# Optimization experiments

Hardware: AMD Instinct MI355X
Metric: run time of the kernel (lower is better)

Reference implementation:

```python
import jax, jax.numpy as jnp
import numpy as np

VN, BN, NSW, EC, MN = 64, 200, 10, 63, 73
FIN, HID = 32, 64
VLOW, VUPP = 0.9, 1.1


def _ln(z, eps=1e-5):
    m = jnp.mean(z, axis=-1, keepdims=True)
    v = jnp.var(z, axis=-1, keepdims=True)
    return (z - m) * jax.lax.rsqrt(v + eps)


def _layer(x, s, conn, deg_inv, Ws, Wi, Wj, U, Vw, first):
    # dense gated edge update over (B,V,V,H)
    e = jnp.einsum('bvwh,hk->bvwk', s, Ws) + (x @ Wi)[:, :, None, :] + (x @ Wj)[:, None, :, :]
    e = jax.nn.relu(_ln(e))
    s_out = e if first else s + e
    gate = jax.nn.sigmoid(s_out) * conn[None, :, :, None]
    msg = jnp.einsum('bvwh,bwh->bvh', gate, x @ Vw) * deg_inv[None, :, None]  # mean agg
    h = jax.nn.relu(_ln(x @ U + msg))
    return (h if first else x + h), s_out


def setup_inputs() -> dict:
    key = jax.random.key(0)
    ks = jax.random.split(key, 24)
    # radial feeder: path graph (line edges) + long-range tie switches, i<j (triu)
    ea = np.stack([np.arange(VN - 1), np.arange(1, VN)]).astype(np.int32)
    es = np.stack([np.arange(NSW), np.arange(NSW) + 32]).astype(np.int32)
    A = np.zeros((VN, VN), np.float32); A[ea[0], ea[1]] = 1; A[ea[1], ea[0]] = 1
    S = np.zeros((VN, VN), np.float32); S[es[0], es[1]] = 1; S[es[1], es[0]] = 1
    par = np.concatenate([ea[0], es[0]]); chi = np.concatenate([ea[1], es[1]])
    Incp = np.zeros((VN, MN), np.float32); Incp[par, np.arange(MN)] = 1
    Incc = np.zeros((VN, MN), np.float32); Incc[chi, np.arange(MN)] = 1
    deg = (A + S).sum(1)
    Dinv = np.diag((1.0 / np.maximum(deg, 1.0)).astype(np.float32))

    def w(k, shape):
        return jax.random.normal(k, shape, jnp.float32) / np.sqrt(shape[-2])

    return {
        'x': jax.random.normal(ks[0], (BN, VN, FIN), jnp.float32),
        'A': jnp.asarray(A), 'S': jnp.asarray(S),
        'embed_s': jax.random.normal(ks[1], (2, FIN), jnp.float32),
        'p0_Ws': w(ks[2], (FIN, HID)), 'p0_Wi': w(ks[3], (FIN, HID)),
        'p0_Wj': w(ks[4], (FIN, HID)), 'p0_U': w(ks[5], (FIN, HID)),
        'p0_V': w(ks[6], (FIN, HID)),
        'pl_Ws': w(ks[7], (2, HID, HID)), 'pl_Wi': w(ks[8], (2, HID, HID)),
        'pl_Wj': w(ks[9], (2, HID, HID)), 'pl_U': w(ks[10], (2, HID, HID)),
        'pl_V': w(ks[11], (2, HID, HID)),
        'smlp_W1': w(ks[12], (4 * HID, 4 * HID)), 'smlp_W2': w(ks[13], (4 * HID, 4)),
        'cmlp_W1': w(ks[14], (3 * HID, 3 * HID)), 'cmlp_W2': w(ks[15], (3 * HID, 3)),
        'Dinv': jnp.asarray(Dinv), 'Incp': jnp.asarray(Incp), 'Incc': jnp.asarray(Incc),
        'edge_A': jnp.asarray(ea), 'edge_S': jnp.asarray(es),
    }


def reference(x, A, S, embed_s, p0_Ws, p0_Wi, p0_Wj, p0_U, p0_V,
              pl_Ws, pl_Wi, pl_Wj, pl_U, pl_V,
              smlp_W1, smlp_W2, cmlp_W1, cmlp_W2,
              Dinv, Incp, Incc, edge_A, edge_S):
    B = x.shape[0]
    conn = jnp.clip(A + S, 0.0, 1.0)                       # (V,V) union adjacency
    deg_inv = 1.0 / jnp.maximum(conn.sum(1), 1.0)
    # init_embed_edges over dense S -> (B,V,V,FIN)
    s = jnp.broadcast_to(embed_s[S.astype(jnp.int32)][None], (B, VN, VN, FIN))
    xh, s = _layer(x, s, conn, deg_inv, p0_Ws, p0_Wi, p0_Wj, p0_U, p0_V, True)
    for l in range(pl_Ws.shape[0]):
        xh, s = _layer(xh, s, conn, deg_inv, pl_Ws[l], pl_Wi[l], pl_Wj[l], pl_U[l], pl_V[l], False)
    x_g = xh.sum(1)                                        # (B,H) graph feature

    # -- switch head (gather at triu switch edges, identical across batch) --
    si, sj = edge_S[0], edge_S[1]
    xg_s = jnp.broadcast_to(x_g[:, None, :], (B, si.shape[0], HID))
    smlp_in = jnp.concatenate([s[:, si, sj, :], xh[:, si], xh[:, sj], xg_s], axis=-1)
    smlp_out = jax.nn.sigmoid(jax.nn.relu(smlp_in @ smlp_W1) @ smlp_W2)  # (B,nsw,4)
    topology = smlp_out[..., 0]
    graph_topo = jnp.concatenate([jnp.ones((B, MN - NSW), x.dtype), topology], axis=1)
    ps = smlp_out[..., 1] - 0.5
    vs_p = VLOW * (1 - smlp_out[..., 2]) + VUPP * smlp_out[..., 2]
    vs_c = VLOW * (1 - smlp_out[..., 3]) + VUPP * smlp_out[..., 3]

    # -- connection head (gather at triu line edges) --
    ai, aj = edge_A[0], edge_A[1]
    xg_c = jnp.broadcast_to(x_g[:, None, :], (B, ai.shape[0], HID))
    cmlp_in = jnp.concatenate([xh[:, ai], xh[:, aj], xg_c], axis=-1)
    cmlp_out = jax.nn.sigmoid(jax.nn.relu(cmlp_in @ cmlp_W1) @ cmlp_W2)  # (B,Ec,3)
    pc = cmlp_out[..., 0] - 0.5
    vc_p = VLOW * (1 - cmlp_out[..., 1]) + VUPP * cmlp_out[..., 1]
    vc_c = VLOW * (1 - cmlp_out[..., 2]) + VUPP * cmlp_out[..., 2]

    # scatter into (B,M) physics tensors: first M-nsw cols from CMLP, last nsw from SMLP
    p_flow = jnp.concatenate([pc, ps], axis=1)
    v_par = jnp.concatenate([vc_p, vs_p], axis=1)
    v_chi = jnp.concatenate([vc_c, vs_c], axis=1)
    v = v_par @ (Dinv @ Incp).T + v_chi @ (Dinv @ Incc).T   # (B,V)
    v = v.at[:, 0].set(1.0)
    return jnp.concatenate([p_flow, v, graph_topo], axis=1)  # (B, M+V+M)
```

## Files before the change

kernel.cpp:

```cpp
#include <hip/hip_runtime.h>

#define BN 200
#define VN 64
#define HIDD 64
#define FINN 32
#define NSW 10
#define EC 63
#define MNE 73
#define NEDGE 146
#define NPACK 256

typedef unsigned short u16;
typedef unsigned int u32;
typedef _Float16 f16;
typedef __attribute__((ext_vector_type(8))) _Float16 f16x8;
typedef __attribute__((ext_vector_type(4))) float f32x4;

__device__ __forceinline__ float bfu(u16 u) { return __uint_as_float(((u32)u) << 16); }
__device__ __forceinline__ u16 f2bf(float f) {
    u32 x = __float_as_uint(f);
    u32 r = x + 0x7fffu + ((x >> 16) & 1u);
    return (u16)(r >> 16);
}
__device__ __forceinline__ float cvtv(const void* p, int i, int fl) {
    return fl ? bfu(((const u16*)p)[i]) : ((const float*)p)[i];
}
__device__ __forceinline__ int rfl(int v) { return __builtin_amdgcn_readfirstlane(v); }

__device__ __forceinline__ int swzp(int row, int col) { return col ^ ((row & 7) << 2); }
__device__ __forceinline__ int swz16(int row, int col) { return col ^ ((row & 7) << 3); }

__device__ __forceinline__ float ldh(const u16* P, int i) {
    union { u16 u; f16 h; } c; c.u = P[i];
    return (float)c.h;
}
__device__ __forceinline__ void sth(u16* P, int i, float f) {
    union { u16 u; f16 h; } c; c.h = (f16)f;
    P[i] = c.u;
}
__device__ __forceinline__ u16 f2h(float f) {
    union { u16 u; f16 h; } c; c.h = (f16)f;
    return c.u;
}
__device__ __forceinline__ f16x8 ldfragh(const u16* P, int i0) {
    return *(const f16x8*)&P[i0];
}

template <int CTRL>
__device__ __forceinline__ float dppadd(float x) {
    int v = __builtin_amdgcn_update_dpp(0, __float_as_int(x), CTRL, 0xf, 0xf, 1);
    return x + __int_as_float(v);
}
__device__ __forceinline__ float rl63(float x) {
    return __int_as_float(__builtin_amdgcn_readlane(__float_as_int(x), 63));
}

__device__ __forceinline__ void ln4_dpp(float ea, float eb, float ec, float ed,
                                        float& ra, float& rb, float& rc, float& rd) {
    float a1 = ea, b1 = eb, c1 = ec, d1 = ed;
    float a2 = ea * ea, b2 = eb * eb, c2 = ec * ec, d2 = ed * ed;
#define LSTEP(C) a1 = dppadd<C>(a1); b1 = dppadd<C>(b1); c1 = dppadd<C>(c1); d1 = dppadd<C>(d1); \
                 a2 = dppadd<C>(a2); b2 = dppadd<C>(b2); c2 = dppadd<C>(c2); d2 = dppadd<C>(d2);
    LSTEP(0x111) LSTEP(0x112) LSTEP(0x114) LSTEP(0x118) LSTEP(0x142) LSTEP(0x143)
#undef LSTEP
    float s1a = rl63(a1), s2a = rl63(a2);
    float s1b = rl63(b1), s2b = rl63(b2);
    float s1c = rl63(c1), s2c = rl63(c2);
    float s1d = rl63(d1), s2d = rl63(d2);
    float ma = s1a * 0.015625f, mb = s1b * 0.015625f;
    float mc = s1c * 0.015625f, md = s1d * 0.015625f;
    float va = fmaxf(s2a * 0.015625f - ma * ma, 0.f);
    float vb = fmaxf(s2b * 0.015625f - mb * mb, 0.f);
    float vc = fmaxf(s2c * 0.015625f - mc * mc, 0.f);
    float vd = fmaxf(s2d * 0.015625f - md * md, 0.f);
    ra = fmaxf((ea - ma) * rsqrtf(va + 1e-5f), 0.f);
    rb = fmaxf((eb - mb) * rsqrtf(vb + 1e-5f), 0.f);
    rc = fmaxf((ec - mc) * rsqrtf(vc + 1e-5f), 0.f);
    rd = fmaxf((ed - md) * rsqrtf(vd + 1e-5f), 0.f);
}

__device__ __forceinline__ float sigm(float x) {
    return __fdividef(1.f, 1.f + __expf(-x));
}

struct CvtArgs { const void* src[21]; };

__global__ __launch_bounds__(256) void k_prep(CvtArgs ca, const int* __restrict__ eA,
                                              const int* __restrict__ eS,
                                              u16* __restrict__ c1p, u16* __restrict__ c2p,
                                              u16* __restrict__ s1p, u16* __restrict__ s2p,
                                              u16* __restrict__ w0p, u16* __restrict__ wlp,
                                              float* __restrict__ ews, float* __restrict__ dinv,
                                              int* __restrict__ row_ptr, int* __restrict__ colp,
                                              int* __restrict__ sw_eidx,
                                              float* __restrict__ dinvD, int* __restrict__ incCnt,
                                              int* __restrict__ incM) {
    int t = threadIdx.x;
    int fl = (((const u16*)ca.src[1])[1] == 0x3F80) ? 1 : 0;
    if (blockIdx.x == 0) {
        __shared__ unsigned char flagL[64 * 65];
        __shared__ float wsL[FINN * 64];
        __shared__ float emL[64];
        __shared__ int degL[64], rpS[65], colS[NEDGE + 16];
        __shared__ int eAL[2 * EC], eSL[2 * NSW];

        if (t < 2 * EC) eAL[t] = eA[t];
        if (t >= 128 && t < 128 + 2 * NSW) eSL[t - 128] = eS[t - 128];
        if (t >= 160 && t < 224) emL[t - 160] = cvtv(ca.src[3], t - 160, fl);
        for (int i = t; i < FINN * 64; i += 256) wsL[i] = cvtv(ca.src[4], i, fl);
        for (int i = t; i < 4096; i += 256) {
            float a = cvtv(ca.src[1], i, fl);
            float s = cvtv(ca.src[2], i, fl);
            int r = i >> 6, c = i & 63;
            flagL[r * 65 + c] = (unsigned char)(((a != 0.f || s != 0.f) ? 1 : 0) |
                                                ((s != 0.f) ? 2 : 0));
        }
        __syncthreads();

        if (t < 128) {
            int j = t >> 6, k = t & 63;
            float a = 0.f;
#pragma unroll
            for (int h = 0; h < FINN; h++) a += emL[j * FINN + h] * wsL[h * 64 + k];
            ews[(j << 6) + k] = a;
        }
        if (t < 64) {
            int d = 0;
#pragma unroll
            for (int w = 0; w < 64; w++) d += flagL[t * 65 + w] & 1;
            degL[t] = d;
            dinv[t] = 1.f / fmaxf((float)d, 1.f);
        }
        __syncthreads();
        if (t == 0) {
            int c = 0;
            for (int v = 0; v < 64; v++) { rpS[v] = c; c += degL[v]; }
            rpS[64] = c;
        }
        __syncthreads();
        if (t < 65) row_ptr[t] = rpS[t];
        if (t < 64) {
            int pos = rpS[t];
#pragma unroll
            for (int w = 0; w < 64; w++) {
                int f = flagL[t * 65 + w];
                if (f & 1) colS[pos++] = w | ((f & 2) ? 256 : 0) | (t << 16);
            }
        }
        __syncthreads();
        int tot = rpS[64];
        if (t < tot) colp[t] = colS[t];
        if (t < NSW) {
            int si = eSL[t], sj = eSL[NSW + t];
            int idx = 0;
            for (int e = rpS[si]; e < rpS[si + 1]; e++)
                if ((colS[e] & 255) == sj) idx = e;
            sw_eidx[t] = idx;
        }
        if (t < 64) {
            dinvD[t] = cvtv(ca.src[18], t * 64 + t, fl);
            int cnt = 0;
            for (int m = 0; m < MNE; m++) {
                int par = (m < EC) ? eAL[m] : eSL[m - EC];
                int chi = (m < EC) ? eAL[EC + m] : eSL[NSW + (m - EC)];
                if (par == t && cnt < 8) incM[t * 8 + cnt++] = (m << 1);
                if (chi == t && cnt < 8) incM[t * 8 + cnt++] = (m << 1) | 1;
            }
            incCnt[t] = cnt;
        }
    } else {
        const int T1 = 36864, T2 = T1 + 3072, T3 = T2 + 65536, T4 = T3 + 4096;
        const int T5 = T4 + 8192, TOT = T5 + 40960;
        for (int i = (blockIdx.x - 1) * 256 + t; i < TOT; i += NPACK * 256) {
            int idx = i;
            const void* src;
            u16* dp;
            int K2, N2, nt, rem, loff = 0;
            if (idx < T1) {
                nt = idx / 3072; rem = idx - nt * 3072; src = ca.src[16];
                dp = c1p + idx; K2 = 192; N2 = 192;
            } else if (idx < T2) {
                idx -= T1; nt = 0; rem = idx; src = ca.src[17];
                dp = c2p + idx; K2 = 192; N2 = 3;
            } else if (idx < T3) {
                idx -= T2; nt = idx >> 12; rem = idx & 4095; src = ca.src[14];
                dp = s1p + idx; K2 = 256; N2 = 256;
            } else if (idx < T4) {
                idx -= T3; nt = 0; rem = idx; src = ca.src[15];
                dp = s2p + idx; K2 = 256; N2 = 4;
            } else if (idx < T5) {
                int j = idx - T4;
                int mt = j >> 11;
                int m2 = j & 2047;
                nt = m2 >> 9; rem = m2 & 511; src = ca.src[5 + mt];
                dp = w0p + j; K2 = 32; N2 = 64;
            } else {
                int j = idx - T5;
                int l = j / 20480;
                int jj = j - l * 20480;
                int mt = jj >> 12;
                int m2 = jj & 4095;
                nt = m2 >> 10; rem = m2 & 1023; src = ca.src[9 + mt];
                loff = l * 4096;
                dp = wlp + j; K2 = 64; N2 = 64;
            }
            int kb = rem >> 9, r8 = rem & 511, ln = r8 >> 3, jq = r8 & 7;
            int k = kb * 32 + ((ln >> 4) << 3) + jq;
            int n = nt * 16 + (ln & 15);
            float val = 0.f;
            if (n < N2 && k < K2) val = cvtv(src, loff + k * N2 + n, fl);
            *dp = f2h(val);
        }
    }
}

#define XI 0
#define XJ 1
#define XU 2
#define XV 3

__global__ __launch_bounds__(1024) void k_main(
    const void* __restrict__ xraw, const u16* __restrict__ A_u16,
    const int* __restrict__ eA, const int* __restrict__ eS,
    const float* __restrict__ ews, const float* __restrict__ dinv,
    const int* __restrict__ row_ptr, const int* __restrict__ colp,
    const int* __restrict__ sw_eidx,
    const float* __restrict__ dinvD, const int* __restrict__ incCnt, const int* __restrict__ incM,
    const u16* __restrict__ w0p, const u16* __restrict__ wlp,
    const u16* __restrict__ c1p, const u16* __restrict__ c2p,
    const u16* __restrict__ s1p, const u16* __restrict__ s2p,
    void* __restrict__ out_v)
{
    __shared__ __align__(16) u16 xPh[64 * 64];
    __shared__ __align__(16) u16 sPh[NEDGE * 64];
    __shared__ __align__(16) float preL[NEDGE * 64];
    __shared__ __align__(16) float tLs[4 * 64 * 64];
    __shared__ __align__(16) u16 xg16[64];
    __shared__ float ewsL[128];
    __shared__ float dinvL[64];
    __shared__ int rpL[65];
    __shared__ int colL[NEDGE + 6];
    __shared__ int swLx[NSW];
    __shared__ int eALs[2 * EC], eSLs[2 * NSW];
    __shared__ float cmoL[EC * 3], smoL[NSW * 4];

    int b = blockIdx.x, t = threadIdx.x;
    int lane = t & 63, wid = t >> 6;
    int m = lane & 15, quad = lane >> 4;
    int fl = (A_u16[1] == 0x3F80) ? 1 : 0;

    for (int i = t; i < 2048; i += 1024) {
        int r = i >> 5, c = i & 31;
        sth(xPh, (r << 6) + swz16(r, c), cvtv(xraw, b * 2048 + i, fl));
    }
    if (t < 128) ewsL[t] = ews[t];
    if (t < 64) dinvL[t] = dinv[t];
    if (t < 65) rpL[t] = row_ptr[t];
    if (t < NEDGE) colL[t] = colp[t];
    if (t < NSW) swLx[t] = sw_eidx[t];
    if (t >= 256 && t < 256 + 2 * EC) eALs[t - 256] = eA[t - 256];
    if (t >= 512 && t < 512 + 2 * NSW) eSLs[t - 512] = eS[t - 512];
    __syncthreads();

    {
        int mat = wid >> 2, Mt = wid & 3;
        const u16* bp = w0p + mat * 2048;
        int row = Mt * 16 + m;
        f16x8 a = ldfragh(xPh, (row << 6) + swz16(row, quad * 8));
        f32x4 acc[4];
#pragma unroll
        for (int nt = 0; nt < 4; nt++) {
            f16x8 bfr = ldfragh(bp, (nt << 9) + (lane << 3));
            acc[nt] = __builtin_amdgcn_mfma_f32_16x16x32_f16(a, bfr, (f32x4){0.f, 0.f, 0.f, 0.f}, 0, 0, 0);
        }
#pragma unroll
        for (int nt = 0; nt < 4; nt++)
#pragma unroll
            for (int r = 0; r < 4; r++) {
                int orow = Mt * 16 + quad * 4 + r;
                tLs[mat * 4096 + (orow << 6) + swzp(orow, nt * 16 + m)] = acc[nt][r];
            }
    }
    __syncthreads();

    for (int base = 0; base < NEDGE; base += 64) {
        int e0 = base + wid;
        int e1i = e0 + 16, e2i = e0 + 32, e3i = e0 + 48;
        int ok1 = e1i < NEDGE, ok2 = e2i < NEDGE, ok3 = e3i < NEDGE;
        int f1 = ok1 ? e1i : e0, f2 = ok2 ? e2i : e0, f3 = ok3 ? e3i : e0;
        int cp0 = rfl(colL[e0]), cp1 = rfl(colL[f1]);
        int cp2 = rfl(colL[f2]), cp3 = rfl(colL[f3]);
        int w0 = cp0 & 255, v0 = (cp0 >> 16) & 255;
        int w1 = cp1 & 255, v1 = (cp1 >> 16) & 255;
        int w2 = cp2 & 255, v2 = (cp2 >> 16) & 255;
        int w3 = cp3 & 255, v3 = (cp3 >> 16) & 255;
        int h0i = (e0 << 6) + swz16(e0, lane);
        int h1i = (f1 << 6) + swz16(f1, lane);
        int h2i = (f2 << 6) + swz16(f2, lane);
        int h3i = (f3 << 6) + swz16(f3, lane);
        int p0i = (e0 << 6) + swzp(e0, lane);
        int p1i = (f1 << 6) + swzp(f1, lane);
        int p2i = (f2 << 6) + swzp(f2, lane);
        int p3i = (f3 << 6) + swzp(f3, lane);
        float ee0 = ewsL[(((cp0 >> 8) & 1) << 6) + lane]
                  + tLs[XI * 4096 + (v0 << 6) + swzp(v0, lane)]
                  + tLs[XJ * 4096 + (w0 << 6) + swzp(w0, lane)];
        float ee1 = ewsL[(((cp1 >> 8) & 1) << 6) + lane]
                  + tLs[XI * 4096 + (v1 << 6) + swzp(v1, lane)]
                  + tLs[XJ * 4096 + (w1 << 6) + swzp(w1, lane)];
        float ee2 = ewsL[(((cp2 >> 8) & 1) << 6) + lane]
                  + tLs[XI * 4096 + (v2 << 6) + swzp(v2, lane)]
                  + tLs[XJ * 4096 + (w2 << 6) + swzp(w2, lane)];
        float ee3 = ewsL[(((cp3 >> 8) & 1) << 6) + lane]
                  + tLs[XI * 4096 + (v3 << 6) + swzp(v3, lane)]
                  + tLs[XJ * 4096 + (w3 << 6) + swzp(w3, lane)];
        float h0, h1, h2, h3;
        ln4_dpp(ee0, ee1, ee2, ee3, h0, h1, h2, h3);
        sth(sPh, h0i, h0);
        preL[p0i] = tLs[XV * 4096 + (w0 << 6) + swzp(w0, lane)] * sigm(h0);
        if (ok1) {
            sth(sPh, h1i, h1);
            preL[p1i] = tLs[XV * 4096 + (w1 << 6) + swzp(w1, lane)] * sigm(h1);
        }
        if (ok2) {
            sth(sPh, h2i, h2);
            preL[p2i] = tLs[XV * 4096 + (w2 << 6) + swzp(w2, lane)] * sigm(h2);
        }
        if (ok3) {
            sth(sPh, h3i, h3);
            preL[p3i] = tLs[XV * 4096 + (w3 << 6) + swzp(w3, lane)] * sigm(h3);
        }
    }
    __syncthreads();

    {
        int v0 = wid << 2;
        int r0 = rfl(rpL[v0]), r1 = rfl(rpL[v0 + 1]), r2 = rfl(rpL[v0 + 2]);
        int r3 = rfl(rpL[v0 + 3]), r4 = rfl(rpL[v0 + 4]);
        float mc0 = 0.f, mc1 = 0.f, mc2 = 0.f, mc3 = 0.f;
        for (int e = r0; e < r1; e++) mc0 += preL[(e << 6) + swzp(e, lane)];
        for (int e = r1; e < r2; e++) mc1 += preL[(e << 6) + swzp(e, lane)];
        for (int e = r2; e < r3; e++) mc2 += preL[(e << 6) + swzp(e, lane)];
        for (int e = r3; e < r4; e++) mc3 += preL[(e << 6) + swzp(e, lane)];
        float z0 = tLs[XU * 4096 + ((v0 + 0) << 6) + swzp(v0 + 0, lane)] + mc0 * dinvL[v0 + 0];
        float z1 = tLs[XU * 4096 + ((v0 + 1) << 6) + swzp(v0 + 1, lane)] + mc1 * dinvL[v0 + 1];
        float z2 = tLs[XU * 4096 + ((v0 + 2) << 6) + swzp(v0 + 2, lane)] + mc2 * dinvL[v0 + 2];
        float z3 = tLs[XU * 4096 + ((v0 + 3) << 6) + swzp(v0 + 3, lane)] + mc3 * dinvL[v0 + 3];
        float h0, h1, h2, h3;
        ln4_dpp(z0, z1, z2, z3, h0, h1, h2, h3);
        sth(xPh, ((v0 + 0) << 6) + swz16(v0 + 0, lane), h0);
        sth(xPh, ((v0 + 1) << 6) + swz16(v0 + 1, lane), h1);
        sth(xPh, ((v0 + 2) << 6) + swz16(v0 + 2, lane), h2);
        sth(xPh, ((v0 + 3) << 6) + swz16(v0 + 3, lane), h3);
    }
    __syncthreads();

    for (int l = 0; l < 2; l++) {
        {
            int mat = wid >> 2, Mt = wid & 3;
            const u16* bp = wlp + l * 20480 + (mat + 1) * 4096;
            int row = Mt * 16 + m;
            f32x4 acc[4];
#pragma unroll
            for (int nt = 0; nt < 4; nt++) acc[nt] = (f32x4){0.f, 0.f, 0.f, 0.f};
#pragma unroll
            for (int kb = 0; kb < 2; kb++) {
                f16x8 a = ldfragh(xPh, (row << 6) + swz16(row, kb * 32 + quad * 8));
#pragma unroll
                for (int nt = 0; nt < 4; nt++) {
                    f16x8 bfr = ldfragh(bp, (((nt << 1) + kb) << 9) + (lane << 3));
                    acc[nt] = __builtin_amdgcn_mfma_f32_16x16x32_f16(a, bfr, acc[nt], 0, 0, 0);
                }
            }
#pragma unroll
            for (int nt = 0; nt < 4; nt++)
#pragma unroll
                for (int r = 0; r < 4; r++) {
                    int orow = Mt * 16 + quad * 4 + r;
                    tLs[mat * 4096 + (orow << 6) + swzp(orow, nt * 16 + m)] = acc[nt][r];
                }

            const u16* sbp = wlp + l * 20480;
            for (int u = wid; u < 40; u += 16) {
                int rt = u >> 2, ntq = u & 3;
                int srow = rt * 16 + m;
                int ar = (srow > NEDGE - 1) ? (NEDGE - 1) : srow;
                f32x4 sacc = (f32x4){0.f, 0.f, 0.f, 0.f};
#pragma unroll
                for (int kb = 0; kb < 2; kb++) {
                    f16x8 a = ldfragh(sPh, (ar << 6) + swz16(ar, kb * 32 + quad * 8));
                    f16x8 bfr = ldfragh(sbp, (((ntq << 1) + kb) << 9) + (lane << 3));
                    sacc = __builtin_amdgcn_mfma_f32_16x16x32_f16(a, bfr, sacc, 0, 0, 0);
                }
#pragma unroll
                for (int r = 0; r < 4; r++) {
                    int orow = rt * 16 + quad * 4 + r;
                    if (orow < NEDGE)
                        preL[(orow << 6) + swzp(orow, ntq * 16 + m)] = sacc[r];
                }
            }
        }
        __syncthreads();

        for (int base = 0; base < NEDGE; base += 64) {
            int e0 = base + wid;
            int e1i = e0 + 16, e2i = e0 + 32, e3i = e0 + 48;
            int ok1 = e1i < NEDGE, ok2 = e2i < NEDGE, ok3 = e3i < NEDGE;
            int f1 = ok1 ? e1i : e0, f2 = ok2 ? e2i : e0, f3 = ok3 ? e3i : e0;
            int cp0 = rfl(colL[e0]), cp1 = rfl(colL[f1]);
            int cp2 = rfl(colL[f2]), cp3 = rfl(colL[f3]);
            int w0 = cp0 & 255, v0 = (cp0 >> 16) & 255;
            int w1 = cp1 & 255, v1 = (cp1 >> 16) & 255;
            int w2 = cp2 & 255, v2 = (cp2 >> 16) & 255;
            int w3 = cp3 & 255, v3 = (cp3 >> 16) & 255;
            int h0i = (e0 << 6) + swz16(e0, lane);
            int h1i = (f1 << 6) + swz16(f1, lane);
            int h2i = (f2 << 6) + swz16(f2, lane);
            int h3i = (f3 << 6) + swz16(f3, lane);
            int p0i = (e0 << 6) + swzp(e0, lane);
            int p1i = (f1 << 6) + swzp(f1, lane);
            int p2i = (f2 << 6) + swzp(f2, lane);
            int p3i = (f3 << 6) + swzp(f3, lane);
            float ee0 = preL[p0i]
                      + tLs[XI * 4096 + (v0 << 6) + swzp(v0, lane)]
                      + tLs[XJ * 4096 + (w0 << 6) + swzp(w0, lane)];
            float ee1 = preL[p1i]
                      + tLs[XI * 4096 + (v1 << 6) + swzp(v1, lane)]
                      + tLs[XJ * 4096 + (w1 << 6) + swzp(w1, lane)];
            float ee2 = preL[p2i]
                      + tLs[XI * 4096 + (v2 << 6) + swzp(v2, lane)]
                      + tLs[XJ * 4096 + (w2 << 6) + swzp(w2, lane)];
            float ee3 = preL[p3i]
                      + tLs[XI * 4096 + (v3 << 6) + swzp(v3, lane)]
                      + tLs[XJ * 4096 + (w3 << 6) + swzp(w3, lane)];
            float h0, h1, h2, h3;
            ln4_dpp(ee0, ee1, ee2, ee3, h0, h1, h2, h3);
            float s0 = ldh(sPh, h0i) + h0;
            sth(sPh, h0i, s0);
            preL[p0i] = tLs[XV * 4096 + (w0 << 6) + swzp(w0, lane)] * sigm(s0);
            if (ok1) {
                float s1v = ldh(sPh, h1i) + h1;
                sth(sPh, h1i, s1v);
                preL[p1i] = tLs[XV * 4096 + (w1 << 6) + swzp(w1, lane)] * sigm(s1v);
            }
            if (ok2) {
                float s2v = ldh(sPh, h2i) + h2;
                sth(sPh, h2i, s2v);
                preL[p2i] = tLs[XV * 4096 + (w2 << 6) + swzp(w2, lane)] * sigm(s2v);
            }
            if (ok3) {
                float s3v = ldh(sPh, h3i) + h3;
                sth(sPh, h3i, s3v);
                preL[p3i] = tLs[XV * 4096 + (w3 << 6) + swzp(w3, lane)] * sigm(s3v);
            }
        }
        __syncthreads();

        {
            int v0 = wid << 2;
            int r0 = rfl(rpL[v0]), r1 = rfl(rpL[v0 + 1]), r2 = rfl(rpL[v0 + 2]);
            int r3 = rfl(rpL[v0 + 3]), r4 = rfl(rpL[v0 + 4]);
            float mc0 = 0.f, mc1 = 0.f, mc2 = 0.f, mc3 = 0.f;
            for (int e = r0; e < r1; e++) mc0 += preL[(e << 6) + swzp(e, lane)];
            for (int e = r1; e < r2; e++) mc1 += preL[(e << 6) + swzp(e, lane)];
            for (int e = r2; e < r3; e++) mc2 += preL[(e << 6) + swzp(e, lane)];
            for (int e = r3; e < r4; e++) mc3 += preL[(e << 6) + swzp(e, lane)];
            float z0 = tLs[XU * 4096 + ((v0 + 0) << 6) + swzp(v0 + 0, lane)] + mc0 * dinvL[v0 + 0];
            float z1 = tLs[XU * 4096 + ((v0 + 1) << 6) + swzp(v0 + 1, lane)] + mc1 * dinvL[v0 + 1];
            float z2 = tLs[XU * 4096 + ((v0 + 2) << 6) + swzp(v0 + 2, lane)] + mc2 * dinvL[v0 + 2];
            float z3 = tLs[XU * 4096 + ((v0 + 3) << 6) + swzp(v0 + 3, lane)] + mc3 * dinvL[v0 + 3];
            float h0, h1, h2, h3;
            ln4_dpp(z0, z1, z2, z3, h0, h1, h2, h3);
            int i0 = ((v0 + 0) << 6) + swz16(v0 + 0, lane);
            int i1 = ((v0 + 1) << 6) + swz16(v0 + 1, lane);
            int i2 = ((v0 + 2) << 6) + swz16(v0 + 2, lane);
            int i3 = ((v0 + 3) << 6) + swz16(v0 + 3, lane);
            float x0 = ldh(xPh, i0) + h0;
            float x1 = ldh(xPh, i1) + h1;
            float x2 = ldh(xPh, i2) + h2;
            float x3 = ldh(xPh, i3) + h3;
            sth(xPh, i0, x0);
            sth(xPh, i1, x1);
            sth(xPh, i2, x2);
            sth(xPh, i3, x3);
            if (l == 1) tLs[(wid << 6) + lane] = x0 + x1 + x2 + x3;
        }
        __syncthreads();
    }

    if (t < 64) {
        float s = 0.f;
#pragma unroll
        for (int i = 0; i < 16; i++) s += tLs[(i << 6) + t];
        sth(xg16, t, s);
    }
    __syncthreads();

    u16* hcP = (u16*)tLs;
    u16* hsP = (u16*)tLs + 12288;

    if (wid < 12) {
        int Mt = wid & 3, ntg = wid >> 2;
        int e = Mt * 16 + m; if (e > 62) e = 62;
        int ai = eALs[e], aj = eALs[EC + e];
        f32x4 acc[4];
#pragma unroll
        for (int j = 0; j < 4; j++) acc[j] = (f32x4){0.f, 0.f, 0.f, 0.f};
#pragma unroll
        for (int kb = 0; kb < 6; kb++) {
            int k = kb * 32 + quad * 8;
            f16x8 a;
            if (k < 64) {
                a = ldfragh(xPh, (ai << 6) + swz16(ai, k));
            } else if (k < 128) {
                a = ldfragh(xPh, (aj << 6) + swz16(aj, k - 64));
            } else {
                a = ldfragh(xg16, k - 128);
            }
#pragma unroll
            for (int j = 0; j < 4; j++) {
                int nt = ntg * 4 + j;
                f16x8 bfr = ldfragh(c1p, ((nt * 6 + kb) << 9) + (lane << 3));
                acc[j] = __builtin_amdgcn_mfma_f32_16x16x32_f16(a, bfr, acc[j], 0, 0, 0);
            }
        }
#pragma unroll
        for (int j = 0; j < 4; j++) {
            int nt = ntg * 4 + j;
#pragma unroll
            for (int r = 0; r < 4; r++) {
                int row = Mt * 16 + quad * 4 + r;
                sth(hcP, row * 192 + swz16(row, nt * 16 + m), fmaxf(acc[j][r], 0.f));
            }
        }
    } else {
        int e2 = (m > 9) ? 9 : m;
        int si = eSLs[e2], sj = eSLs[NSW + e2];
        int sw = swLx[e2];
        f32x4 accS[4];
#pragma unroll
        for (int j = 0; j < 4; j++) accS[j] = (f32x4){0.f, 0.f, 0.f, 0.f};
#pragma unroll
        for (int kb = 0; kb < 8; kb++) {
            int k = kb * 32 + quad * 8;
            f16x8 a;
            if (k < 64) {
                a = ldfragh(sPh, (sw << 6) + swz16(sw, k));
            } else if (k < 128) {
                a = ldfragh(xPh, (si << 6) + swz16(si, k - 64));
            } else if (k < 192) {
                a = ldfragh(xPh, (sj << 6) + swz16(sj, k - 128));
            } else {
                a = ldfragh(xg16, k - 192);
            }
#pragma unroll
            for (int j = 0; j < 4; j++) {
                int nt = (wid - 12) * 4 + j;
                f16x8 bfr = ldfragh(s1p, ((nt * 8 + kb) << 9) + (lane << 3));
                accS[j] = __builtin_amdgcn_mfma_f32_16x16x32_f16(a, bfr, accS[j], 0, 0, 0);
            }
        }
#pragma unroll
        for (int j = 0; j < 4; j++) {
            int nt = (wid - 12) * 4 + j;
#pragma unroll
            for (int r = 0; r < 4; r++) {
                int row = quad * 4 + r;
                sth(hsP, (row << 8) + swz16(row, nt * 16 + m), fmaxf(accS[j][r], 0.f));
            }
        }
    }
    __syncthreads();

    if (wid < 4) {
        f32x4 accD = (f32x4){0.f, 0.f, 0.f, 0.f};
        int row = wid * 16 + m;
#pragma unroll
        for (int kb = 0; kb < 6; kb++) {
            f16x8 a = ldfragh(hcP, row * 192 + swz16(row, kb * 32 + quad * 8));
            f16x8 bfr = ldfragh(c2p, (kb << 9) + (lane << 3));
            accD = __builtin_amdgcn_mfma_f32_16x16x32_f16(a, bfr, accD, 0, 0, 0);
        }
#pragma unroll
        for (int r = 0; r < 4; r++) {
            int row2 = wid * 16 + quad * 4 + r;
            if (row2 < EC && m < 3)
                cmoL[row2 * 3 + m] = 1.f / (1.f + __expf(-accD[r]));
        }
    } else if (wid == 4) {
        f32x4 accT = (f32x4){0.f, 0.f, 0.f, 0.f};
#pragma unroll
        for (int kb = 0; kb < 8; kb++) {
            f16x8 a = ldfragh(hsP, (m << 8) + swz16(m, kb * 32 + quad * 8));
            f16x8 bfr = ldfragh(s2p, (kb << 9) + (lane << 3));
            accT = __builtin_amdgcn_mfma_f32_16x16x32_f16(a, bfr, accT, 0, 0, 0);
        }
#pragma unroll
        for (int r = 0; r < 4; r++) {
            int row = quad * 4 + r;
            if (row < NSW && m < 4)
                smoL[row * 4 + m] = 1.f / (1.f + __expf(-accT[r]));
        }
    }
    __syncthreads();

    if (t < 2 * MNE + VN) {
        float val;
        if (t < MNE) {
            val = (t < EC) ? cmoL[t * 3] - 0.5f : smoL[(t - EC) * 4 + 1] - 0.5f;
        } else if (t < MNE + VN) {
            int i = t - MNE;
            if (i == 0) {
                val = 1.0f;
            } else {
                float acc = 0.f;
                int c = incCnt[i];
                for (int q = 0; q < c; q++) {
                    int em = incM[i * 8 + q];
                    int mm = em >> 1, role = em & 1;
                    float vv = (mm < EC) ? 0.9f + 0.2f * cmoL[mm * 3 + 1 + role]
                                         : 0.9f + 0.2f * smoL[(mm - EC) * 4 + 2 + role];
                    acc += vv;
                }
                val = acc * dinvD[i];
            }
        } else {
            int mm = t - (MNE + VN);
            val = (mm < EC) ? 1.0f : smoL[(mm - EC) * 4];
        }
        size_t oidx = (size_t)b * (2 * MNE + VN) + t;
        if (fl) ((u16*)out_v)[oidx] = f2bf(val);
        else    ((float*)out_v)[oidx] = val;
    }
}

extern "C" void kernel_launch(void* const* d_in, const int* in_sizes, int n_in,
                              void* d_out, int out_size, void* d_ws, size_t ws_size,
                              hipStream_t stream) {
    const int* eA = (const int*)d_in[21];
    const int* eS = (const int*)d_in[22];

    float* pool = (float*)d_ws;
    float* ews     = pool;
    float* dinv    = ews + 128;
    float* dinvD   = dinv + 64;
    int*   row_ptr = (int*)(dinvD + 64);
    int*   colp    = row_ptr + 80;
    int*   sw_eidx = colp + 256;
    int*   incCnt  = sw_eidx + 16;
    int*   incM    = incCnt + 64;
    u16*   c1p = (u16*)(incM + 512);
    u16*   c2p = c1p + 36864;
    u16*   s1p = c2p + 3072;
    u16*   s2p = s1p + 65536;
    u16*   w0p = s2p + 4096;
    u16*   wlp = w0p + 8192;

    CvtArgs ca;
    for (int i = 0; i < 21; i++) ca.src[i] = d_in[i];

    k_prep<<<1 + NPACK, 256, 0, stream>>>(ca, eA, eS,
                                          c1p, c2p, s1p, s2p, w0p, wlp,
                                          ews, dinv, row_ptr, colp, sw_eidx,
                                          dinvD, incCnt, incM);

    k_main<<<BN, 1024, 0, stream>>>(d_in[0], (const u16*)d_in[1], eA, eS,
                                    ews, dinv, row_ptr, colp, sw_eidx,
                                    dinvD, incCnt, incM,
                                    w0p, wlp, c1p, c2p, s1p, s2p,
                                    d_out);
}
```

Baseline: 152.7 us.

## Process two channels per lane with half-wave edges and paired DPP layernorm

```diff
diff --git a/kernel.cpp b/kernel.cpp
--- a/kernel.cpp
+++ b/kernel.cpp
@@ -25,7 +25,6 @@
 __device__ __forceinline__ float cvtv(const void* p, int i, int fl) {
     return fl ? bfu(((const u16*)p)[i]) : ((const float*)p)[i];
 }
-__device__ __forceinline__ int rfl(int v) { return __builtin_amdgcn_readfirstlane(v); }
 
 __device__ __forceinline__ int swzp(int row, int col) { return col ^ ((row & 7) << 2); }
 __device__ __forceinline__ int swz16(int row, int col) { return col ^ ((row & 7) << 3); }
@@ -40,6 +39,14 @@
 }
 __device__ __forceinline__ u16 f2h(float f) {
     union { u16 u; f16 h; } c; c.h = (f16)f;
+    return c.u;
+}
+__device__ __forceinline__ void unp2(u32 w, float& a, float& b) {
+    union { u32 u; f16 h[2]; } c; c.u = w;
+    a = (float)c.h[0]; b = (float)c.h[1];
+}
+__device__ __forceinline__ u32 pk2(float a, float b) {
+    union { u32 u; f16 h[2]; } c; c.h[0] = (f16)a; c.h[1] = (f16)b;
     return c.u;
 }
 __device__ __forceinline__ f16x8 ldfragh(const u16* P, int i0) {
@@ -51,32 +58,27 @@
     int v = __builtin_amdgcn_update_dpp(0, __float_as_int(x), CTRL, 0xf, 0xf, 1);
     return x + __int_as_float(v);
 }
-__device__ __forceinline__ float rl63(float x) {
-    return __int_as_float(__builtin_amdgcn_readlane(__float_as_int(x), 63));
-}
-
-__device__ __forceinline__ void ln4_dpp(float ea, float eb, float ec, float ed,
-                                        float& ra, float& rb, float& rc, float& rd) {
-    float a1 = ea, b1 = eb, c1 = ec, d1 = ed;
-    float a2 = ea * ea, b2 = eb * eb, c2 = ec * ec, d2 = ed * ed;
-#define LSTEP(C) a1 = dppadd<C>(a1); b1 = dppadd<C>(b1); c1 = dppadd<C>(c1); d1 = dppadd<C>(d1); \
-                 a2 = dppadd<C>(a2); b2 = dppadd<C>(b2); c2 = dppadd<C>(c2); d2 = dppadd<C>(d2);
-    LSTEP(0x111) LSTEP(0x112) LSTEP(0x114) LSTEP(0x118) LSTEP(0x142) LSTEP(0x143)
-#undef LSTEP
-    float s1a = rl63(a1), s2a = rl63(a2);
-    float s1b = rl63(b1), s2b = rl63(b2);
-    float s1c = rl63(c1), s2c = rl63(c2);
-    float s1d = rl63(d1), s2d = rl63(d2);
-    float ma = s1a * 0.015625f, mb = s1b * 0.015625f;
-    float mc = s1c * 0.015625f, md = s1d * 0.015625f;
-    float va = fmaxf(s2a * 0.015625f - ma * ma, 0.f);
-    float vb = fmaxf(s2b * 0.015625f - mb * mb, 0.f);
-    float vc = fmaxf(s2c * 0.015625f - mc * mc, 0.f);
-    float vd = fmaxf(s2d * 0.015625f - md * md, 0.f);
-    ra = fmaxf((ea - ma) * rsqrtf(va + 1e-5f), 0.f);
-    rb = fmaxf((eb - mb) * rsqrtf(vb + 1e-5f), 0.f);
-    rc = fmaxf((ec - mc) * rsqrtf(vc + 1e-5f), 0.f);
-    rd = fmaxf((ed - md) * rsqrtf(vd + 1e-5f), 0.f);
+template <int N>
+__device__ __forceinline__ float rlN(float x) {
+    return __int_as_float(__builtin_amdgcn_readlane(__float_as_int(x), N));
+}
+
+__device__ __forceinline__ void lnpair(float p0, float p1, int isHi, float& o0, float& o1) {
+    float s1 = p0 + p1;
+    float s2 = fmaf(p0, p0, p1 * p1);
+    s1 = dppadd<0x111>(s1); s1 = dppadd<0x112>(s1); s1 = dppadd<0x114>(s1); s1 = dppadd<0x118>(s1);
+    s2 = dppadd<0x111>(s2); s2 = dppadd<0x112>(s2); s2 = dppadd<0x114>(s2); s2 = dppadd<0x118>(s2);
+    float a1 = rlN<15>(s1) + rlN<31>(s1);
+    float b1 = rlN<47>(s1) + rlN<63>(s1);
+    float a2 = rlN<15>(s2) + rlN<31>(s2);
+    float b2 = rlN<47>(s2) + rlN<63>(s2);
+    float S1 = isHi ? b1 : a1;
+    float S2 = isHi ? b2 : a2;
+    float mean = S1 * 0.015625f;
+    float var = fmaxf(S2 * 0.015625f - mean * mean, 0.f);
+    float rn = rsqrtf(var + 1e-5f);
+    o0 = fmaxf((p0 - mean) * rn, 0.f);
+    o1 = fmaxf((p1 - mean) * rn, 0.f);
 }
 
 __device__ __forceinline__ float sigm(float x) {
@@ -247,11 +249,22 @@
     int b = blockIdx.x, t = threadIdx.x;
     int lane = t & 63, wid = t >> 6;
     int m = lane & 15, quad = lane >> 4;
+    int half = lane >> 5, hl = lane & 31, c2 = hl << 1;
     int fl = (A_u16[1] == 0x3F80) ? 1 : 0;
 
-    for (int i = t; i < 2048; i += 1024) {
-        int r = i >> 5, c = i & 31;
-        sth(xPh, (r << 6) + swz16(r, c), cvtv(xraw, b * 2048 + i, fl));
+    {
+        int i2 = t << 1;
+        int r = i2 >> 5, c = i2 & 31;
+        float va, vb;
+        if (fl) {
+            u32 wv = ((const u32*)xraw)[(size_t)b * 1024 + t];
+            va = bfu((u16)(wv & 0xffffu));
+            vb = bfu((u16)(wv >> 16));
+        } else {
+            float2 f = ((const float2*)xraw)[(size_t)b * 1024 + t];
+            va = f.x; vb = f.y;
+        }
+        *(u32*)&xPh[(r << 6) + swz16(r, c)] = pk2(va, vb);
     }
     if (t < 128) ewsL[t] = ews[t];
     if (t < 64) dinvL[t] = dinv[t];
@@ -283,75 +296,51 @@
     }
     __syncthreads();
 
-    for (int base = 0; base < NEDGE; base += 64) {
-        int e0 = base + wid;
-        int e1i = e0 + 16, e2i = e0 + 32, e3i = e0 + 48;
-        int ok1 = e1i < NEDGE, ok2 = e2i < NEDGE, ok3 = e3i < NEDGE;
-        int f1 = ok1 ? e1i : e0, f2 = ok2 ? e2i : e0, f3 = ok3 ? e3i : e0;
-        int cp0 = rfl(colL[e0]), cp1 = rfl(colL[f1]);
-        int cp2 = rfl(colL[f2]), cp3 = rfl(colL[f3]);
-        int w0 = cp0 & 255, v0 = (cp0 >> 16) & 255;
-        int w1 = cp1 & 255, v1 = (cp1 >> 16) & 255;
-        int w2 = cp2 & 255, v2 = (cp2 >> 16) & 255;
-        int w3 = cp3 & 255, v3 = (cp3 >> 16) & 255;
-        int h0i = (e0 << 6) + swz16(e0, lane);
-        int h1i = (f1 << 6) + swz16(f1, lane);
-        int h2i = (f2 << 6) + swz16(f2, lane);
-        int h3i = (f3 << 6) + swz16(f3, lane);
-        int p0i = (e0 << 6) + swzp(e0, lane);
-        int p1i = (f1 << 6) + swzp(f1, lane);
-        int p2i = (f2 << 6) + swzp(f2, lane);
-        int p3i = (f3 << 6) + swzp(f3, lane);
-        float ee0 = ewsL[(((cp0 >> 8) & 1) << 6) + lane]
-                  + tLs[XI * 4096 + (v0 << 6) + swzp(v0, lane)]
-                  + tLs[XJ * 4096 + (w0 << 6) + swzp(w0, lane)];
-        float ee1 = ewsL[(((cp1 >> 8) & 1) << 6) + lane]
-                  + tLs[XI * 4096 + (v1 << 6) + swzp(v1, lane)]
-                  + tLs[XJ * 4096 + (w1 << 6) + swzp(w1, lane)];
-        float ee2 = ewsL[(((cp2 >> 8) & 1) << 6) + lane]
-                  + tLs[XI * 4096 + (v2 << 6) + swzp(v2, lane)]
-                  + tLs[XJ * 4096 + (w2 << 6) + swzp(w2, lane)];
-        float ee3 = ewsL[(((cp3 >> 8) & 1) << 6) + lane]
-                  + tLs[XI * 4096 + (v3 << 6) + swzp(v3, lane)]
-                  + tLs[XJ * 4096 + (w3 << 6) + swzp(w3, lane)];
-        float h0, h1, h2, h3;
-        ln4_dpp(ee0, ee1, ee2, ee3, h0, h1, h2, h3);
-        sth(sPh, h0i, h0);
-        preL[p0i] = tLs[XV * 4096 + (w0 << 6) + swzp(w0, lane)] * sigm(h0);
-        if (ok1) {
-            sth(sPh, h1i, h1);
-            preL[p1i] = tLs[XV * 4096 + (w1 << 6) + swzp(w1, lane)] * sigm(h1);
-        }
-        if (ok2) {
-            sth(sPh, h2i, h2);
-            preL[p2i] = tLs[XV * 4096 + (w2 << 6) + swzp(w2, lane)] * sigm(h2);
-        }
-        if (ok3) {
-            sth(sPh, h3i, h3);
-            preL[p3i] = tLs[XV * 4096 + (w3 << 6) + swzp(w3, lane)] * sigm(h3);
+    for (int base = 0; base < NEDGE; base += 128) {
+#pragma unroll
+        for (int s = 0; s < 4; s++) {
+            int q = (s << 1) + half;
+            int e = base + wid + (q << 4);
+            int ok = e < NEDGE;
+            int ec = ok ? e : (NEDGE - 1);
+            int cp = colL[ec];
+            int w = cp & 255, v = (cp >> 16) & 255;
+            float2 ew = *(const float2*)&ewsL[((((cp >> 8) & 1)) << 6) + c2];
+            float2 xi = *(const float2*)&tLs[XI * 4096 + (v << 6) + swzp(v, c2)];
+            float2 xj = *(const float2*)&tLs[XJ * 4096 + (w << 6) + swzp(w, c2)];
+            float p0 = ew.x + xi.x + xj.x;
+            float p1 = ew.y + xi.y + xj.y;
+            float h0, h1;
+            lnpair(p0, p1, half, h0, h1);
+            float2 xv = *(const float2*)&tLs[XV * 4096 + (w << 6) + swzp(w, c2)];
+            float2 g;
+            g.x = xv.x * sigm(h0);
+            g.y = xv.y * sigm(h1);
+            if (ok) {
+                *(u32*)&sPh[(ec << 6) + swz16(ec, c2)] = pk2(h0, h1);
+                *(float2*)&preL[(ec << 6) + swzp(ec, c2)] = g;
+            }
         }
     }
     __syncthreads();
 
     {
-        int v0 = wid << 2;
-        int r0 = rfl(rpL[v0]), r1 = rfl(rpL[v0 + 1]), r2 = rfl(rpL[v0 + 2]);
-        int r3 = rfl(rpL[v0 + 3]), r4 = rfl(rpL[v0 + 4]);
-        float mc0 = 0.f, mc1 = 0.f, mc2 = 0.f, mc3 = 0.f;
-        for (int e = r0; e < r1; e++) mc0 += preL[(e << 6) + swzp(e, lane)];
-        for (int e = r1; e < r2; e++) mc1 += preL[(e << 6) + swzp(e, lane)];
-        for (int e = r2; e < r3; e++) mc2 += preL[(e << 6) + swzp(e, lane)];
-        for (int e = r3; e < r4; e++) mc3 += preL[(e << 6) + swzp(e, lane)];
-        float z0 = tLs[XU * 4096 + ((v0 + 0) << 6) + swzp(v0 + 0, lane)] + mc0 * dinvL[v0 + 0];
-        float z1 = tLs[XU * 4096 + ((v0 + 1) << 6) + swzp(v0 + 1, lane)] + mc1 * dinvL[v0 + 1];
-        float z2 = tLs[XU * 4096 + ((v0 + 2) << 6) + swzp(v0 + 2, lane)] + mc2 * dinvL[v0 + 2];
-        float z3 = tLs[XU * 4096 + ((v0 + 3) << 6) + swzp(v0 + 3, lane)] + mc3 * dinvL[v0 + 3];
-        float h0, h1, h2, h3;
-        ln4_dpp(z0, z1, z2, z3, h0, h1, h2, h3);
-        sth(xPh, ((v0 + 0) << 6) + swz16(v0 + 0, lane), h0);
-        sth(xPh, ((v0 + 1) << 6) + swz16(v0 + 1, lane), h1);
-        sth(xPh, ((v0 + 2) << 6) + swz16(v0 + 2, lane), h2);
-        sth(xPh, ((v0 + 3) << 6) + swz16(v0 + 3, lane), h3);
+#pragma unroll
+        for (int s = 0; s < 2; s++) {
+            int v = (wid << 2) + (s << 1) + half;
+            int r0 = rpL[v], r1 = rpL[v + 1];
+            float m0 = 0.f, m1 = 0.f;
+            for (int e = r0; e < r1; e++) {
+                float2 p = *(const float2*)&preL[(e << 6) + swzp(e, c2)];
+                m0 += p.x; m1 += p.y;
+            }
+            float2 xu = *(const float2*)&tLs[XU * 4096 + (v << 6) + swzp(v, c2)];
+            float di = dinvL[v];
+            float z0 = xu.x + m0 * di, z1 = xu.y + m1 * di;
+            float h0, h1;
+            lnpair(z0, z1, half, h0, h1);
+            *(u32*)&xPh[(v << 6) + swz16(v, c2)] = pk2(h0, h1);
+        }
     }
     __syncthreads();
 
@@ -402,88 +391,65 @@
         }
         __syncthreads();
 
-        for (int base = 0; base < NEDGE; base += 64) {
-            int e0 = base + wid;
-            int e1i = e0 + 16, e2i = e0 + 32, e3i = e0 + 48;
-            int ok1 = e1i < NEDGE, ok2 = e2i < NEDGE, ok3 = e3i < NEDGE;
-            int f1 = ok1 ? e1i : e0, f2 = ok2 ? e2i : e0, f3 = ok3 ? e3i : e0;
-            int cp0 = rfl(colL[e0]), cp1 = rfl(colL[f1]);
-            int cp2 = rfl(colL[f2]), cp3 = rfl(colL[f3]);
-            int w0 = cp0 & 255, v0 = (cp0 >> 16) & 255;
-            int w1 = cp1 & 255, v1 = (cp1 >> 16) & 255;
-            int w2 = cp2 & 255, v2 = (cp2 >> 16) & 255;
-            int w3 = cp3 & 255, v3 = (cp3 >> 16) & 255;
-            int h0i = (e0 << 6) + swz16(e0, lane);
-            int h1i = (f1 << 6) + swz16(f1, lane);
-            int h2i = (f2 << 6) + swz16(f2, lane);
-            int h3i = (f3 << 6) + swz16(f3, lane);
-            int p0i = (e0 << 6) + swzp(e0, lane);
-            int p1i = (f1 << 6) + swzp(f1, lane);
-            int p2i = (f2 << 6) + swzp(f2, lane);
-            int p3i = (f3 << 6) + swzp(f3, lane);
-            float ee0 = preL[p0i]
-                      + tLs[XI * 4096 + (v0 << 6) + swzp(v0, lane)]
-                      + tLs[XJ * 4096 + (w0 << 6) + swzp(w0, lane)];
-            float ee1 = preL[p1i]
-                      + tLs[XI * 4096 + (v1 << 6) + swzp(v1, lane)]
-                      + tLs[XJ * 4096 + (w1 << 6) + swzp(w1, lane)];
-            float ee2 = preL[p2i]
-                      + tLs[XI * 4096 + (v2 << 6) + swzp(v2, lane)]
-                      + tLs[XJ * 4096 + (w2 << 6) + swzp(w2, lane)];
-            float ee3 = preL[p3i]
-                      + tLs[XI * 4096 + (v3 << 6) + swzp(v3, lane)]
-                      + tLs[XJ * 4096 + (w3 << 6) + swzp(w3, lane)];
-            float h0, h1, h2, h3;
-            ln4_dpp(ee0, ee1, ee2, ee3, h0, h1, h2, h3);
-            float s0 = ldh(sPh, h0i) + h0;
-            sth(sPh, h0i, s0);
-            preL[p0i] = tLs[XV * 4096 + (w0 << 6) + swzp(w0, lane)] * sigm(s0);
-            if (ok1) {
-                float s1v = ldh(sPh, h1i) + h1;
-                sth(sPh, h1i, s1v);
-                preL[p1i] = tLs[XV * 4096 + (w1 << 6) + swzp(w1, lane)] * sigm(s1v);
-            }
-            if (ok2) {
-                float s2v = ldh(sPh, h2i) + h2;
-                sth(sPh, h2i, s2v);
-                preL[p2i] = tLs[XV * 4096 + (w2 << 6) + swzp(w2, lane)] * sigm(s2v);
-            }
-            if (ok3) {
-                float s3v = ldh(sPh, h3i) + h3;
-                sth(sPh, h3i, s3v);
-                preL[p3i] = tLs[XV * 4096 + (w3 << 6) + swzp(w3, lane)] * sigm(s3v);
+        for (int base = 0; base < NEDGE; base += 128) {
+#pragma unroll
+            for (int s = 0; s < 4; s++) {
+                int q = (s << 1) + half;
+                int e = base + wid + (q << 4);
+                int ok = e < NEDGE;
+                int ec = ok ? e : (NEDGE - 1);
+                int cp = colL[ec];
+                int w = cp & 255, v = (cp >> 16) & 255;
+                int pidx = (ec << 6) + swzp(ec, c2);
+                float2 pre = *(const float2*)&preL[pidx];
+                float2 xi = *(const float2*)&tLs[XI * 4096 + (v << 6) + swzp(v, c2)];
+                float2 xj = *(const float2*)&tLs[XJ * 4096 + (w << 6) + swzp(w, c2)];
+                float p0 = pre.x + xi.x + xj.x;
+                float p1 = pre.y + xi.y + xj.y;
+                float h0, h1;
+                lnpair(p0, p1, half, h0, h1);
+                int hidx = (ec << 6) + swz16(ec, c2);
+                float so0, so1;
+                unp2(*(const u32*)&sPh[hidx], so0, so1);
+                float n0 = so0 + h0, n1 = so1 + h1;
+                float2 xv = *(const float2*)&tLs[XV * 4096 + (w << 6) + swzp(w, c2)];
+                float2 g;
+                g.x = xv.x * sigm(n0);
+                g.y = xv.y * sigm(n1);
+                if (ok) {
+                    *(u32*)&sPh[hidx] = pk2(n0, n1);
+                    *(float2*)&preL[pidx] = g;
+                }
             }
         }
         __syncthreads();
 
         {
-            int v0 = wid << 2;
-            int r0 = rfl(rpL[v0]), r1 = rfl(rpL[v0 + 1]), r2 = rfl(rpL[v0 + 2]);
-            int r3 = rfl(rpL[v0 + 3]), r4 = rfl(rpL[v0 + 4]);
-            float mc0 = 0.f, mc1 = 0.f, mc2 = 0.f, mc3 = 0.f;
-            for (int e = r0; e < r1; e++) mc0 += preL[(e << 6) + swzp(e, lane)];
-            for (int e = r1; e < r2; e++) mc1 += preL[(e << 6) + swzp(e, lane)];
-            for (int e = r2; e < r3; e++) mc2 += preL[(e << 6) + swzp(e, lane)];
-            for (int e = r3; e < r4; e++) mc3 += preL[(e << 6) + swzp(e, lane)];
-            float z0 = tLs[XU * 4096 + ((v0 + 0) << 6) + swzp(v0 + 0, lane)] + mc0 * dinvL[v0 + 0];
-            float z1 = tLs[XU * 4096 + ((v0 + 1) << 6) + swzp(v0 + 1, lane)] + mc1 * dinvL[v0 + 1];
-            float z2 = tLs[XU * 4096 + ((v0 + 2) << 6) + swzp(v0 + 2, lane)] + mc2 * dinvL[v0 + 2];
-            float z3 = tLs[XU * 4096 + ((v0 + 3) << 6) + swzp(v0 + 3, lane)] + mc3 * dinvL[v0 + 3];
-            float h0, h1, h2, h3;
-            ln4_dpp(z0, z1, z2, z3, h0, h1, h2, h3);
-            int i0 = ((v0 + 0) << 6) + swz16(v0 + 0, lane);
-            int i1 = ((v0 + 1) << 6) + swz16(v0 + 1, lane);
-            int i2 = ((v0 + 2) << 6) + swz16(v0 + 2, lane);
-            int i3 = ((v0 + 3) << 6) + swz16(v0 + 3, lane);
-            float x0 = ldh(xPh, i0) + h0;
-            float x1 = ldh(xPh, i1) + h1;
-            float x2 = ldh(xPh, i2) + h2;
-            float x3 = ldh(xPh, i3) + h3;
-            sth(xPh, i0, x0);
-            sth(xPh, i1, x1);
-            sth(xPh, i2, x2);
-            sth(xPh, i3, x3);
-            if (l == 1) tLs[(wid << 6) + lane] = x0 + x1 + x2 + x3;
+            float xa0 = 0.f, xa1 = 0.f;
+#pragma unroll
+            for (int s = 0; s < 2; s++) {
+                int v = (wid << 2) + (s << 1) + half;
+                int r0 = rpL[v], r1 = rpL[v + 1];
+                float m0 = 0.f, m1 = 0.f;
+                for (int e = r0; e < r1; e++) {
+                    float2 p = *(const float2*)&preL[(e << 6) + swzp(e, c2)];
+                    m0 += p.x; m1 += p.y;
+                }
+                float2 xu = *(const float2*)&tLs[XU * 4096 + (v << 6) + swzp(v, c2)];
+                float di = dinvL[v];
+                float z0 = xu.x + m0 * di, z1 = xu.y + m1 * di;
+                float h0, h1;
+                lnpair(z0, z1, half, h0, h1);
+                int xi16 = (v << 6) + swz16(v, c2);
+                float o0, o1;
+                unp2(*(const u32*)&xPh[xi16], o0, o1);
+                float x0 = o0 + h0, x1 = o1 + h1;
+                *(u32*)&xPh[xi16] = pk2(x0, x1);
+                xa0 += x0; xa1 += x1;
+            }
+            if (l == 1) {
+                *(float2*)&tLs[(wid << 7) + (half << 6) + c2] = make_float2(xa0, xa1);
+            }
         }
         __syncthreads();
     }
@@ -491,7 +457,8 @@
     if (t < 64) {
         float s = 0.f;
 #pragma unroll
-        for (int i = 0; i < 16; i++) s += tLs[(i << 6) + t];
+        for (int i = 0; i < 16; i++)
+            s += tLs[(i << 7) + t] + tLs[(i << 7) + 64 + t];
         sth(xg16, t, s);
     }
     __syncthreads();
```

New measurement: 149.0 us. 1.02x faster.
